# Kernel optimization log

Hardware: AMD Instinct MI355X
Metric: run time of the kernel (lower is better)

## Reference

```python
import jax, jax.numpy as jnp
import numpy as np

N_NODES = 100_000
N_EDGES = 3_200_000
WEIGHT_LIMIT = 5000.0
RIDGE = 1e-7


def _polynomial_basis(diff):
    # diff: [E, 2] -> [E, 5] basis (x, y, x*y, x^2, y^2)
    x = diff[:, 0]
    y = diff[:, 1]
    return jnp.stack([x, y, x * y, x * x, y * y], axis=-1)


def setup_inputs() -> dict:
    key = jax.random.key(0)
    k1, k2, k3 = jax.random.split(key, 3)
    pos = jax.random.normal(k1, (N_NODES, 2), dtype=jnp.float32)
    row = jax.random.randint(k2, (N_EDGES,), 0, N_NODES, dtype=jnp.int64)
    col = jax.random.randint(k3, (N_EDGES,), 0, N_NODES, dtype=jnp.int64)
    edge_index = jnp.stack([row, col], axis=0)
    return {"pos": pos, "edge_index": edge_index}


def reference(pos, edge_index):
    # With a dense random graph, 2-hop extension adds no edges, so the
    # augmented edge_index equals the original edge_index.
    row = edge_index[0]
    col = edge_index[1]
    n = pos.shape[0]

    # Edge displacement (detached in the original module).
    diff = jax.lax.stop_gradient(pos[col] - pos[row])  # [E, 2]
    H = _polynomial_basis(diff).astype(jnp.float32)    # [E, 5]

    # Per-edge outer products, scatter-accumulated per source node.
    M_edge = H[:, :, None] * H[:, None, :]                          # [E, 5, 5]
    M_node = jax.ops.segment_sum(M_edge, row, num_segments=n)      # [N, 5, 5]
    M_node = M_node + RIDGE * jnp.eye(5, dtype=jnp.float32)

    # Laplacian RHS: [0, 0, 0, 2, 2] per node (coefficients of x^2, y^2).
    L = jnp.zeros((n, 5), dtype=jnp.float32).at[:, 3:].set(2.0)

    # C = M^{-1} L (per-node 5x5 solve).
    C = jnp.linalg.solve(M_node, L[..., None])[..., 0]              # [N, 5]

    # Per-edge Laplacian weights.
    weights = jnp.sum(C[row] * H, axis=1)                           # [E]
    return jnp.clip(weights, -WEIGHT_LIMIT, WEIGHT_LIMIT)
```

## Files before the change

### kernel.cpp

```cpp
#include <hip/hip_runtime.h>
#include <math.h>

constexpr float WLIM = 5000.0f;
constexpr double RIDGE = 1e-7;

#define G 256
#define MAXNB 1024
#define BN 128
#define CAP 6144
#define EBUF_CAP 12544

__global__ __launch_bounds__(1024) void k_sort(const int* __restrict__ row,
                                               const int* __restrict__ col,
                                               int* __restrict__ table,
                                               unsigned int* __restrict__ sorted,
                                               int nE, int CE, int NB) {
    __shared__ int h[MAXNB];
    __shared__ int t[MAXNB];
    __shared__ unsigned int ebuf[EBUF_CAP];
    const int g = blockIdx.x, tid = threadIdx.x;
    const int NBP = NB + 1;
    const int s = g * CE;
    const int e_end = min(s + CE, nE);
    const int cnt = e_end - s;

    for (int i = tid; i < MAXNB; i += 1024) h[i] = 0;
    __syncthreads();
    for (int i = s + tid; i < e_end; i += 1024)
        atomicAdd(&h[row[i] >> 7], 1);
    __syncthreads();
    int v = h[tid];
    t[tid] = v;
    __syncthreads();
    for (int d = 1; d < MAXNB; d <<= 1) {
        int u = (tid >= d) ? t[tid - d] : 0;
        __syncthreads();
        t[tid] += u;
        __syncthreads();
    }
    int excl = t[tid] - v;
    if (tid < NB) {
        table[(size_t)g * NBP + tid] = excl;
        h[tid] = excl;
    }
    if (tid == 0) table[(size_t)g * NBP + NB] = cnt;
    __syncthreads();
    for (int i = s + tid; i < e_end; i += 1024) {
        int r = row[i];
        int c = col[i];
        int b = r >> 7;
        int p = atomicAdd(&h[b], 1);
        ebuf[p] = ((unsigned)(r & 127) << 17) | (unsigned)c;
    }
    __syncthreads();
    for (int i = tid; i < cnt; i += 1024)
        sorted[s + i] = ebuf[i];
}

__global__ __launch_bounds__(256) void k_node3(const float2* __restrict__ pos,
                                               const unsigned int* __restrict__ sorted,
                                               const int* __restrict__ table,
                                               float* __restrict__ rec,
                                               int nN, int CE, int NB, int nG) {
    __shared__ unsigned int ebuf[CAP];
    __shared__ unsigned int ecol[CAP];
    __shared__ int off[BN + 1];
    __shared__ int cur[BN];
    __shared__ int goff0[G], gplaced[G], glen[G];
    __shared__ int wt[4];
    __shared__ int ovf;
    const int b = blockIdx.x, tid = threadIdx.x;
    const int NBP = NB + 1;

    int off0 = 0, len = 0;
    if (tid < nG) {
        const int* trow = table + (size_t)tid * NBP;
        off0 = trow[b];
        len = trow[b + 1] - off0;
    }
    const int lane = tid & 63, wid = tid >> 6;
    int x = len;
    #pragma unroll
    for (int d = 1; d < 64; d <<= 1) {
        int u = __shfl_up(x, d);
        if (lane >= d) x += u;
    }
    if (lane == 63) wt[wid] = x;
    if (tid == 0) ovf = 0;
    __syncthreads();
    int add = 0;
    #pragma unroll
    for (int w = 0; w < 4; ++w) if (w < wid) add += wt[w];
    int mystart = x + add - len;
    int total = 0;
    {
        __shared__ int tot_s;
        if (tid == 255) tot_s = x + add;
        __syncthreads();
        total = tot_s;
    }
    int placed = min(len, max(0, CAP - mystart));
    if (placed < len) atomicOr(&ovf, 1);
    goff0[tid] = off0; gplaced[tid] = placed; glen[tid] = len;
    int gbase = tid * CE + off0;
    for (int j = 0; j < placed; ++j)
        ebuf[mystart + j] = sorted[gbase + j];
    if (tid < BN + 1) off[tid] = 0;
    __syncthreads();

    const int cntE = min(total, CAP);
    for (int i = tid; i < cntE; i += 256) atomicAdd(&off[(ebuf[i] >> 17) + 1], 1);
    __syncthreads();
    if (tid == 0) {
        int a = 0;
        for (int i = 0; i <= BN; ++i) { a += off[i]; off[i] = a; }
    }
    __syncthreads();
    if (tid < BN) cur[tid] = off[tid];
    __syncthreads();
    for (int i = tid; i < cntE; i += 256) {
        unsigned v = ebuf[i];
        int lr = (int)(v >> 17);
        int p = atomicAdd(&cur[lr], 1);
        ecol[p] = v & 0x1FFFFu;
    }
    __syncthreads();

    if (tid < BN) {
        int n = (b << 7) + tid;
        if (n < nN) {
            float2 pr = pos[n];
            float m[15];
            #pragma unroll
            for (int i = 0; i < 15; ++i) m[i] = 0.0f;
            int j0 = off[tid], j1 = off[tid + 1];
            for (int j = j0; j < j1; ++j) {
                float2 pc = pos[ecol[j]];
                float x2 = pc.x - pr.x;
                float y2 = pc.y - pr.y;
                float xy = x2 * y2, xx = x2 * x2, yy = y2 * y2;
                m[0]  += x2 * x2;  m[1]  += x2 * y2;  m[2]  += x2 * xy; m[3]  += x2 * xx; m[4]  += x2 * yy;
                m[5]  += y2 * y2;  m[6]  += y2 * xy;  m[7]  += y2 * xx; m[8]  += y2 * yy;
                m[9]  += xy * xy;  m[10] += xy * xx;  m[11] += xy * yy;
                m[12] += xx * xx;  m[13] += xx * yy;
                m[14] += yy * yy;
            }
            if (ovf) {
                for (int g2 = 0; g2 < nG; ++g2) {
                    int base2 = g2 * CE + goff0[g2];
                    for (int j = gplaced[g2]; j < glen[g2]; ++j) {
                        unsigned v = sorted[base2 + j];
                        if ((int)(v >> 17) == tid) {
                            float2 pc = pos[v & 0x1FFFFu];
                            float x2 = pc.x - pr.x;
                            float y2 = pc.y - pr.y;
                            float xy = x2 * y2, xx = x2 * x2, yy = y2 * y2;
                            m[0]  += x2 * x2;  m[1]  += x2 * y2;  m[2]  += x2 * xy; m[3]  += x2 * xx; m[4]  += x2 * yy;
                            m[5]  += y2 * y2;  m[6]  += y2 * xy;  m[7]  += y2 * xx; m[8]  += y2 * yy;
                            m[9]  += xy * xy;  m[10] += xy * xx;  m[11] += xy * yy;
                            m[12] += xx * xx;  m[13] += xx * yy;
                            m[14] += yy * yy;
                        }
                    }
                }
            }

            double A[5][5];
            {
                int idx = 0;
                #pragma unroll
                for (int i = 0; i < 5; ++i) {
                    #pragma unroll
                    for (int j = i; j < 5; ++j) {
                        double vv = (double)m[idx++];
                        A[i][j] = vv;
                        A[j][i] = vv;
                    }
                }
            }
            #pragma unroll
            for (int i = 0; i < 5; ++i) A[i][i] += RIDGE;

            #pragma unroll
            for (int k = 0; k < 5; ++k) {
                double d = A[k][k];
                d = sqrt(fmax(d, 1e-300));
                A[k][k] = d;
                double inv = 1.0 / d;
                #pragma unroll
                for (int i = k + 1; i < 5; ++i) A[i][k] *= inv;
                #pragma unroll
                for (int j = k + 1; j < 5; ++j) {
                    #pragma unroll
                    for (int i = j; i < 5; ++i) A[i][j] -= A[i][k] * A[j][k];
                }
            }
            double bb[5] = {0.0, 0.0, 0.0, 2.0, 2.0};
            double y[5];
            #pragma unroll
            for (int i = 0; i < 5; ++i) {
                double sv = bb[i];
                #pragma unroll
                for (int k = 0; k < 5; ++k) {
                    if (k < i) sv -= A[i][k] * y[k];
                }
                y[i] = sv / A[i][i];
            }
            double xs[5];
            #pragma unroll
            for (int ii = 4; ii >= 0; --ii) {
                double sv = y[ii];
                #pragma unroll
                for (int k = 0; k < 5; ++k) {
                    if (k > ii) sv -= A[k][ii] * xs[k];
                }
                xs[ii] = sv / A[ii][ii];
            }
            float4* rb = (float4*)(rec + (size_t)n * 8);
            rb[0] = make_float4((float)xs[0], (float)xs[1], (float)xs[2], (float)xs[3]);
            rb[1] = make_float4((float)xs[4], pr.x, pr.y, 0.0f);
        }
    }
}

__global__ __launch_bounds__(256) void k_weights(const float2* __restrict__ pos,
                                                 const int* __restrict__ row,
                                                 const int* __restrict__ col,
                                                 const float* __restrict__ rec,
                                                 float* __restrict__ out,
                                                 int nE) {
    int e = blockIdx.x * blockDim.x + threadIdx.x;
    if (e >= nE) return;
    int r = row[e];
    int c = col[e];
    const float4* rb = (const float4*)(rec + (size_t)r * 8);
    float4 r0 = rb[0];
    float4 r1 = rb[1];
    float2 pc = pos[c];
    float x = pc.x - r1.y;
    float y = pc.y - r1.z;
    float w = r0.x * x + r0.y * y + r0.z * (x * y) + r0.w * (x * x) + r1.x * (y * y);
    w = fminf(fmaxf(w, -WLIM), WLIM);
    out[e] = w;
}

extern "C" void kernel_launch(void* const* d_in, const int* in_sizes, int n_in,
                              void* d_out, int out_size, void* d_ws, size_t ws_size,
                              hipStream_t stream) {
    const float2* pos = (const float2*)d_in[0];
    const int* ei = (const int*)d_in[1];
    const int nN = in_sizes[0] / 2;
    const int nE = in_sizes[1] / 2;
    const int* row = ei;
    const int* col = ei + nE;

    const int NB = (nN + BN - 1) >> 7;
    const int CE = (nE + G - 1) / G;

    int* table = (int*)d_ws;
    size_t roff = (((size_t)G * (NB + 1)) + 3) & ~(size_t)3;
    float* rec = (float*)((int*)d_ws + roff);

    unsigned int* sorted = (unsigned int*)d_out;
    float* out = (float*)d_out;

    k_sort<<<G, 1024, 0, stream>>>(row, col, table, sorted, nE, CE, NB);
    k_node3<<<NB, 256, 0, stream>>>(pos, sorted, table, rec, nN, CE, NB, G);
    k_weights<<<(nE + 255) / 256, 256, 0, stream>>>(pos, row, col, rec, out, nE);
}
```

Before: 102.0 us.

## Transpose offset table, drop staging buffer, split each node across two threads

The offset table is now stored bucket-major, so each node block reads its per-group offsets with coalesced loads and no longer needs a prefix scan. The node kernel skips the intermediate shared copy of each group's edges. Instead it counts and scatters straight from the sorted global array, which frees one shared buffer and lowers the capacity. Each node is now handled by two threads that split its edges and merge their partial moments with a lane shuffle, so all 256 threads do accumulation work. The cost is that the sorted array is read twice, and blocks that exceed capacity fall back to a slow full rescan.

```diff
diff --git a/kernel.cpp b/kernel.cpp
--- a/kernel.cpp
+++ b/kernel.cpp
@@ -7,7 +7,7 @@
 #define G 256
 #define MAXNB 1024
 #define BN 128
-#define CAP 6144
+#define CAP 5120
 #define EBUF_CAP 12544
 
 __global__ __launch_bounds__(1024) void k_sort(const int* __restrict__ row,
@@ -19,7 +19,6 @@
     __shared__ int t[MAXNB];
     __shared__ unsigned int ebuf[EBUF_CAP];
     const int g = blockIdx.x, tid = threadIdx.x;
-    const int NBP = NB + 1;
     const int s = g * CE;
     const int e_end = min(s + CE, nE);
     const int cnt = e_end - s;
@@ -40,10 +39,10 @@
     }
     int excl = t[tid] - v;
     if (tid < NB) {
-        table[(size_t)g * NBP + tid] = excl;
+        table[(size_t)tid * G + g] = excl;
         h[tid] = excl;
     }
-    if (tid == 0) table[(size_t)g * NBP + NB] = cnt;
+    if (tid == 0) table[(size_t)NB * G + g] = cnt;
     __syncthreads();
     for (int i = s + tid; i < e_end; i += 1024) {
         int r = row[i];
@@ -61,165 +60,143 @@
                                                const unsigned int* __restrict__ sorted,
                                                const int* __restrict__ table,
                                                float* __restrict__ rec,
-                                               int nN, int CE, int NB, int nG) {
+                                               int nN, int CE, int NB) {
     __shared__ unsigned int ebuf[CAP];
-    __shared__ unsigned int ecol[CAP];
     __shared__ int off[BN + 1];
     __shared__ int cur[BN];
-    __shared__ int goff0[G], gplaced[G], glen[G];
-    __shared__ int wt[4];
-    __shared__ int ovf;
+    __shared__ int goff0[G], glen[G];
     const int b = blockIdx.x, tid = threadIdx.x;
-    const int NBP = NB + 1;
-
-    int off0 = 0, len = 0;
-    if (tid < nG) {
-        const int* trow = table + (size_t)tid * NBP;
-        off0 = trow[b];
-        len = trow[b + 1] - off0;
-    }
-    const int lane = tid & 63, wid = tid >> 6;
-    int x = len;
-    #pragma unroll
-    for (int d = 1; d < 64; d <<= 1) {
-        int u = __shfl_up(x, d);
-        if (lane >= d) x += u;
-    }
-    if (lane == 63) wt[wid] = x;
-    if (tid == 0) ovf = 0;
-    __syncthreads();
-    int add = 0;
-    #pragma unroll
-    for (int w = 0; w < 4; ++w) if (w < wid) add += wt[w];
-    int mystart = x + add - len;
-    int total = 0;
-    {
-        __shared__ int tot_s;
-        if (tid == 255) tot_s = x + add;
-        __syncthreads();
-        total = tot_s;
-    }
-    int placed = min(len, max(0, CAP - mystart));
-    if (placed < len) atomicOr(&ovf, 1);
-    goff0[tid] = off0; gplaced[tid] = placed; glen[tid] = len;
-    int gbase = tid * CE + off0;
-    for (int j = 0; j < placed; ++j)
-        ebuf[mystart + j] = sorted[gbase + j];
+
+    int off0 = table[(size_t)b * G + tid];
+    int off1 = table[(size_t)(b + 1) * G + tid];
+    int len = off1 - off0;
+    goff0[tid] = off0; glen[tid] = len;
     if (tid < BN + 1) off[tid] = 0;
     __syncthreads();
 
-    const int cntE = min(total, CAP);
-    for (int i = tid; i < cntE; i += 256) atomicAdd(&off[(ebuf[i] >> 17) + 1], 1);
+    const int gbase = tid * CE + off0;
+    for (int j = 0; j < len; ++j)
+        atomicAdd(&off[(sorted[gbase + j] >> 17) + 1], 1);
     __syncthreads();
     if (tid == 0) {
         int a = 0;
         for (int i = 0; i <= BN; ++i) { a += off[i]; off[i] = a; }
     }
     __syncthreads();
+    const int total = off[BN];
     if (tid < BN) cur[tid] = off[tid];
     __syncthreads();
-    for (int i = tid; i < cntE; i += 256) {
-        unsigned v = ebuf[i];
-        int lr = (int)(v >> 17);
-        int p = atomicAdd(&cur[lr], 1);
-        ecol[p] = v & 0x1FFFFu;
-    }
-    __syncthreads();
-
-    if (tid < BN) {
-        int n = (b << 7) + tid;
-        if (n < nN) {
-            float2 pr = pos[n];
-            float m[15];
-            #pragma unroll
-            for (int i = 0; i < 15; ++i) m[i] = 0.0f;
-            int j0 = off[tid], j1 = off[tid + 1];
-            for (int j = j0; j < j1; ++j) {
-                float2 pc = pos[ecol[j]];
-                float x2 = pc.x - pr.x;
-                float y2 = pc.y - pr.y;
-                float xy = x2 * y2, xx = x2 * x2, yy = y2 * y2;
-                m[0]  += x2 * x2;  m[1]  += x2 * y2;  m[2]  += x2 * xy; m[3]  += x2 * xx; m[4]  += x2 * yy;
-                m[5]  += y2 * y2;  m[6]  += y2 * xy;  m[7]  += y2 * xx; m[8]  += y2 * yy;
-                m[9]  += xy * xy;  m[10] += xy * xx;  m[11] += xy * yy;
-                m[12] += xx * xx;  m[13] += xx * yy;
+
+    const bool fits = (total <= CAP);
+    if (fits) {
+        for (int j = 0; j < len; ++j) {
+            unsigned v = sorted[gbase + j];
+            int p = atomicAdd(&cur[(int)(v >> 17)], 1);
+            ebuf[p] = v & 0x1FFFFu;
+        }
+    }
+    __syncthreads();
+
+    const int node = tid >> 1;
+    const int half = tid & 1;
+    const int n = (b << 7) + node;
+    float m[15];
+    #pragma unroll
+    for (int i = 0; i < 15; ++i) m[i] = 0.0f;
+    float2 pr = make_float2(0.f, 0.f);
+    if (n < nN) {
+        pr = pos[n];
+        if (fits) {
+            int j0 = off[node], j1 = off[node + 1];
+            for (int j = j0 + half; j < j1; j += 2) {
+                float2 pc = pos[ebuf[j]];
+                float x = pc.x - pr.x;
+                float y = pc.y - pr.y;
+                float xy = x * y, xx = x * x, yy = y * y;
+                m[0]  += x * x;   m[1]  += x * y;   m[2]  += x * xy;  m[3]  += x * xx;  m[4]  += x * yy;
+                m[5]  += y * y;   m[6]  += y * xy;  m[7]  += y * xx;  m[8]  += y * yy;
+                m[9]  += xy * xy; m[10] += xy * xx; m[11] += xy * yy;
+                m[12] += xx * xx; m[13] += xx * yy;
                 m[14] += yy * yy;
             }
-            if (ovf) {
-                for (int g2 = 0; g2 < nG; ++g2) {
-                    int base2 = g2 * CE + goff0[g2];
-                    for (int j = gplaced[g2]; j < glen[g2]; ++j) {
-                        unsigned v = sorted[base2 + j];
-                        if ((int)(v >> 17) == tid) {
-                            float2 pc = pos[v & 0x1FFFFu];
-                            float x2 = pc.x - pr.x;
-                            float y2 = pc.y - pr.y;
-                            float xy = x2 * y2, xx = x2 * x2, yy = y2 * y2;
-                            m[0]  += x2 * x2;  m[1]  += x2 * y2;  m[2]  += x2 * xy; m[3]  += x2 * xx; m[4]  += x2 * yy;
-                            m[5]  += y2 * y2;  m[6]  += y2 * xy;  m[7]  += y2 * xx; m[8]  += y2 * yy;
-                            m[9]  += xy * xy;  m[10] += xy * xx;  m[11] += xy * yy;
-                            m[12] += xx * xx;  m[13] += xx * yy;
-                            m[14] += yy * yy;
-                        }
+        } else {
+            for (int g2 = half; g2 < G; g2 += 2) {
+                int base2 = g2 * CE + goff0[g2];
+                for (int j = 0; j < glen[g2]; ++j) {
+                    unsigned v = sorted[base2 + j];
+                    if ((int)(v >> 17) == node) {
+                        float2 pc = pos[v & 0x1FFFFu];
+                        float x = pc.x - pr.x;
+                        float y = pc.y - pr.y;
+                        float xy = x * y, xx = x * x, yy = y * y;
+                        m[0]  += x * x;   m[1]  += x * y;   m[2]  += x * xy;  m[3]  += x * xx;  m[4]  += x * yy;
+                        m[5]  += y * y;   m[6]  += y * xy;  m[7]  += y * xx;  m[8]  += y * yy;
+                        m[9]  += xy * xy; m[10] += xy * xx; m[11] += xy * yy;
+                        m[12] += xx * xx; m[13] += xx * yy;
+                        m[14] += yy * yy;
                     }
                 }
             }
-
-            double A[5][5];
-            {
-                int idx = 0;
+        }
+    }
+    #pragma unroll
+    for (int i = 0; i < 15; ++i) m[i] += __shfl_xor(m[i], 1);
+
+    if (half == 0 && n < nN) {
+        double A[5][5];
+        {
+            int idx = 0;
+            #pragma unroll
+            for (int i = 0; i < 5; ++i) {
                 #pragma unroll
-                for (int i = 0; i < 5; ++i) {
-                    #pragma unroll
-                    for (int j = i; j < 5; ++j) {
-                        double vv = (double)m[idx++];
-                        A[i][j] = vv;
-                        A[j][i] = vv;
-                    }
+                for (int j = i; j < 5; ++j) {
+                    double vv = (double)m[idx++];
+                    A[i][j] = vv;
+                    A[j][i] = vv;
                 }
             }
-            #pragma unroll
-            for (int i = 0; i < 5; ++i) A[i][i] += RIDGE;
-
+        }
+        #pragma unroll
+        for (int i = 0; i < 5; ++i) A[i][i] += RIDGE;
+
+        #pragma unroll
+        for (int k = 0; k < 5; ++k) {
+            double d = A[k][k];
+            d = sqrt(fmax(d, 1e-300));
+            A[k][k] = d;
+            double inv = 1.0 / d;
+            #pragma unroll
+            for (int i = k + 1; i < 5; ++i) A[i][k] *= inv;
+            #pragma unroll
+            for (int j = k + 1; j < 5; ++j) {
+                #pragma unroll
+                for (int i = j; i < 5; ++i) A[i][j] -= A[i][k] * A[j][k];
+            }
+        }
+        double bb[5] = {0.0, 0.0, 0.0, 2.0, 2.0};
+        double y[5];
+        #pragma unroll
+        for (int i = 0; i < 5; ++i) {
+            double sv = bb[i];
             #pragma unroll
             for (int k = 0; k < 5; ++k) {
-                double d = A[k][k];
-                d = sqrt(fmax(d, 1e-300));
-                A[k][k] = d;
-                double inv = 1.0 / d;
-                #pragma unroll
-                for (int i = k + 1; i < 5; ++i) A[i][k] *= inv;
-                #pragma unroll
-                for (int j = k + 1; j < 5; ++j) {
-                    #pragma unroll
-                    for (int i = j; i < 5; ++i) A[i][j] -= A[i][k] * A[j][k];
-                }
-            }
-            double bb[5] = {0.0, 0.0, 0.0, 2.0, 2.0};
-            double y[5];
-            #pragma unroll
-            for (int i = 0; i < 5; ++i) {
-                double sv = bb[i];
-                #pragma unroll
-                for (int k = 0; k < 5; ++k) {
-                    if (k < i) sv -= A[i][k] * y[k];
-                }
-                y[i] = sv / A[i][i];
-            }
-            double xs[5];
-            #pragma unroll
-            for (int ii = 4; ii >= 0; --ii) {
-                double sv = y[ii];
-                #pragma unroll
-                for (int k = 0; k < 5; ++k) {
-                    if (k > ii) sv -= A[k][ii] * xs[k];
-                }
-                xs[ii] = sv / A[ii][ii];
-            }
-            float4* rb = (float4*)(rec + (size_t)n * 8);
-            rb[0] = make_float4((float)xs[0], (float)xs[1], (float)xs[2], (float)xs[3]);
-            rb[1] = make_float4((float)xs[4], pr.x, pr.y, 0.0f);
-        }
+                if (k < i) sv -= A[i][k] * y[k];
+            }
+            y[i] = sv / A[i][i];
+        }
+        double xs[5];
+        #pragma unroll
+        for (int ii = 4; ii >= 0; --ii) {
+            double sv = y[ii];
+            #pragma unroll
+            for (int k = 0; k < 5; ++k) {
+                if (k > ii) sv -= A[k][ii] * xs[k];
+            }
+            xs[ii] = sv / A[ii][ii];
+        }
+        float4* rb = (float4*)(rec + (size_t)n * 8);
+        rb[0] = make_float4((float)xs[0], (float)xs[1], (float)xs[2], (float)xs[3]);
+        rb[1] = make_float4((float)xs[4], pr.x, pr.y, 0.0f);
     }
 }
 
@@ -258,13 +235,13 @@
     const int CE = (nE + G - 1) / G;
 
     int* table = (int*)d_ws;
-    size_t roff = (((size_t)G * (NB + 1)) + 3) & ~(size_t)3;
+    size_t roff = (((size_t)(NB + 1) * G) + 3) & ~(size_t)3;
     float* rec = (float*)((int*)d_ws + roff);
 
     unsigned int* sorted = (unsigned int*)d_out;
     float* out = (float*)d_out;
 
     k_sort<<<G, 1024, 0, stream>>>(row, col, table, sorted, nE, CE, NB);
-    k_node3<<<NB, 256, 0, stream>>>(pos, sorted, table, rec, nN, CE, NB, G);
+    k_node3<<<NB, 256, 0, stream>>>(pos, sorted, table, rec, nN, CE, NB);
     k_weights<<<(nE + 255) / 256, 256, 0, stream>>>(pos, row, col, rec, out, nE);
 }
```

New measurement: 92.52 us. 9.3% less time.
